# Kernel tuning notes

Hardware: AMD Instinct MI355X
Metric: run time of the kernel (lower is better)

## Reference

```python
import jax, jax.numpy as jnp
import numpy as np


def setup_inputs() -> dict:
    key = jax.random.key(0)
    ks = jax.random.split(key, 4)
    T, B, E = 2048, 2, 1024
    query = jax.random.normal(ks[0], (T, B, E), dtype=jnp.float32)
    attn_mask = jnp.zeros((T, T), dtype=jnp.float32)
    Wqkv = jax.random.normal(ks[1], (3 * E, E), dtype=jnp.float32) * 0.02
    bqkv = jnp.zeros((3 * E,), dtype=jnp.float32)
    Wout = jax.random.normal(ks[2], (E, E), dtype=jnp.float32) * 0.02
    bout = jnp.zeros((E,), dtype=jnp.float32)
    return {"query": query, "attn_mask": attn_mask, "Wqkv": Wqkv,
            "bqkv": bqkv, "Wout": Wout, "bout": bout, "num_heads": 16}


def reference(query, attn_mask, Wqkv, bqkv, Wout, bout, num_heads):
    T, B, E = query.shape
    H = num_heads
    hd = E // H
    scaling = hd ** -0.5
    # fused QKV projection: [T,B,3E]
    qkv = jnp.einsum('tbe,fe->tbf', query, Wqkv) + bqkv
    q, k, v = jnp.split(qkv, 3, axis=-1)
    q = q * scaling
    # [T,B,E] -> [B*H, T, hd]
    def to_heads(x):
        return x.reshape(T, B * H, hd).transpose(1, 0, 2)
    q, k, v = to_heads(q), to_heads(k), to_heads(v)
    # scores [B*H, T, T]
    scores = jnp.einsum('bth,bsh->bts', q, k) + attn_mask[None, :, :]
    probs = jax.nn.softmax(scores, axis=-1)  # dropout p=0
    attn = jnp.einsum('bts,bsh->bth', probs, v)  # [B*H, T, hd]
    attn = attn.transpose(1, 0, 2).reshape(T, B, E)
    out = jnp.einsum('tbe,fe->tbf', attn, Wout) + bout
    avg_w = probs.reshape(B, H, T, T).sum(axis=1) / H
    return out, avg_w
```

## Files before the change

### kernel.cpp

```cpp
#include <hip/hip_runtime.h>
#include <cstdint>
#include <cstddef>

#define Tt 2048
#define Bb 2
#define Ee 1024
#define Hh 16
#define HD 64
#define BHh (Bb*Hh)
#define Mm (Tt*Bb)

typedef short bf16x8 __attribute__((ext_vector_type(8)));
typedef float f32x4  __attribute__((ext_vector_type(4)));

#define MFMA16(a,b,c) __builtin_amdgcn_mfma_f32_16x16x32_bf16(a, b, c, 0, 0, 0)

__device__ __forceinline__ unsigned short f2bf(float f) {
    unsigned int u = __builtin_bit_cast(unsigned int, f);
    u += 0x7FFFu + ((u >> 16) & 1u);
    return (unsigned short)(u >> 16);
}
__device__ __forceinline__ unsigned int pack2bf(float lo, float hi) {
    return (unsigned int)f2bf(lo) | ((unsigned int)f2bf(hi) << 16);
}

__device__ __forceinline__ int swzA(int row, int dwcol) {
    return (row*32 + dwcol) ^ ((row & 7) << 2);
}
__device__ __forceinline__ int swzG(int row, int dwcol) {
    return (row*16 + dwcol) ^ ((row & 3) << 2);
}

__device__ __forceinline__ bf16x8 ldfrag(const unsigned short* base, int row, int col) {
    const unsigned int* p = (const unsigned int*)(base + row*66 + col);
    const unsigned int* q = (const unsigned int*)(base + row*66 + col + 16);
    uint4 u;
    u.x = p[0]; u.y = p[1];
    u.z = q[0]; u.w = q[1];
    return __builtin_bit_cast(bf16x8, u);
}

__global__ __launch_bounds__(256)
void to_bf16(const float* __restrict__ src, unsigned short* __restrict__ dst, int n8)
{
    const int stride = gridDim.x * 256;
    for (int i = blockIdx.x*256 + threadIdx.x; i < n8; i += stride) {
        const float4 a = ((const float4*)src)[2*i];
        const float4 b = ((const float4*)src)[2*i + 1];
        const uint4 u = {pack2bf(a.x,a.y), pack2bf(a.z,a.w),
                         pack2bf(b.x,b.y), pack2bf(b.z,b.w)};
        ((uint4*)dst)[i] = u;
    }
}

template<int MODE>
__global__ __launch_bounds__(256)
void gemm_mfma(const unsigned short* __restrict__ A, const unsigned short* __restrict__ W,
               const float* __restrict__ bias, float* __restrict__ Cout,
               unsigned short* __restrict__ qbuf, unsigned short* __restrict__ kbuf,
               unsigned short* __restrict__ vbuf, int N, int K)
{
    __shared__ __align__(16) unsigned int AsDW[128*16];
    __shared__ __align__(16) unsigned int WsDW[128*16];
    const int tid  = threadIdx.x;
    const int bm   = blockIdx.y * 128;
    const int bn   = blockIdx.x * 128;
    const int w    = tid >> 6;
    const int lane = tid & 63;
    const int lr   = lane & 15;
    const int lg   = lane >> 4;
    const int wm   = (w >> 1) * 64;
    const int wn   = (w & 1) * 64;

    f32x4 acc[4][4];
#pragma unroll
    for (int m = 0; m < 4; ++m)
#pragma unroll
        for (int n = 0; n < 4; ++n)
            acc[m][n] = f32x4{0.f, 0.f, 0.f, 0.f};

    const int r1  = tid >> 2;
    const int cdw = (tid & 3) * 4;

    for (int k0 = 0; k0 < K; k0 += 32) {
        __syncthreads();
        {
            const uint4 a0 = *(const uint4*)&A[(size_t)(bm + r1)      * K + k0 + cdw*2];
            const uint4 a1 = *(const uint4*)&A[(size_t)(bm + r1 + 64) * K + k0 + cdw*2];
            const uint4 w0 = *(const uint4*)&W[(size_t)(bn + r1)      * K + k0 + cdw*2];
            const uint4 w1 = *(const uint4*)&W[(size_t)(bn + r1 + 64) * K + k0 + cdw*2];
            *(uint4*)(AsDW + swzG(r1,      cdw)) = a0;
            *(uint4*)(AsDW + swzG(r1 + 64, cdw)) = a1;
            *(uint4*)(WsDW + swzG(r1,      cdw)) = w0;
            *(uint4*)(WsDW + swzG(r1 + 64, cdw)) = w1;
        }
        __syncthreads();

        bf16x8 af[4], wf[4];
#pragma unroll
        for (int i = 0; i < 4; ++i) {
            af[i] = __builtin_bit_cast(bf16x8, *(const uint4*)(AsDW + swzG(wm + 16*i + lr, 4*lg)));
            wf[i] = __builtin_bit_cast(bf16x8, *(const uint4*)(WsDW + swzG(wn + 16*i + lr, 4*lg)));
        }
#pragma unroll
        for (int m = 0; m < 4; ++m)
#pragma unroll
            for (int n = 0; n < 4; ++n)
                acc[m][n] = MFMA16(af[m], wf[n], acc[m][n]);
    }

#pragma unroll
    for (int nsub = 0; nsub < 4; ++nsub) {
        const int n0 = bn + wn + 16*nsub + lr;
        const float bv = bias[n0];
#pragma unroll
        for (int msub = 0; msub < 4; ++msub) {
#pragma unroll
            for (int reg = 0; reg < 4; ++reg) {
                const int m = bm + wm + 16*msub + 4*lg + reg;
                float v = acc[msub][nsub][reg] + bv;
                if (MODE == 0) {
                    const int which = n0 >> 10;
                    const int e0 = n0 & 1023;
                    const int h = e0 >> 6, d0 = e0 & 63;
                    if (which == 0) v *= 0.125f;
                    unsigned short* dst = (which == 0) ? qbuf : (which == 1) ? kbuf : vbuf;
                    dst[((size_t)((m & 1)*Hh + h) * Tt + (m >> 1)) * HD + d0] = f2bf(v);
                } else {
                    Cout[(size_t)m * N + n0] = v;
                }
            }
        }
    }
}

__global__ __launch_bounds__(512)
void attn_mfma(const unsigned short* __restrict__ qb, const unsigned short* __restrict__ kb,
               const unsigned short* __restrict__ vb, const float* __restrict__ mask,
               unsigned short* __restrict__ attnb, float* __restrict__ lbuf)
{
    __shared__ __align__(16) unsigned int KsDW[2][64*32];
    __shared__ __align__(16) unsigned short Vt[2][64*66];
    __shared__ float l_sh[128];

    const int tid  = threadIdx.x;
    const int bid  = blockIdx.x;
    const int wid  = (bid & 7) * 64 + (bid >> 3);
    const int bh   = wid & 31;
    const int t0   = (wid >> 5) * 128;
    const int w    = tid >> 6;
    const int lane = tid & 63;
    const int lr   = lane & 15;
    const int lg   = lane >> 4;
    const int b = bh >> 4, h = bh & 15;

    const unsigned short* __restrict__ Qg = qb + (size_t)bh * Tt * HD;
    const unsigned short* __restrict__ Kg = kb + (size_t)bh * Tt * HD;
    const unsigned short* __restrict__ Vg = vb + (size_t)bh * Tt * HD;

    const int str = tid >> 3;
    const int sdw = (tid & 7) * 4;

    const int vdg = tid & 15;
    const int vs2 = tid >> 4;

    bf16x8 qf[2];
    for (int half = 0; half < 2; ++half) {
        __syncthreads();
        *(uint4*)(KsDW[0] + swzA(str, sdw)) =
            *(const uint4*)&Qg[(size_t)(t0 + half*64 + str) * HD + sdw*2];
        __syncthreads();
        if ((w >> 2) == half) {
            const int r = 16*(w & 3) + lr;
            qf[0] = __builtin_bit_cast(bf16x8, *(const uint4*)(KsDW[0] + swzA(r, 4*lg)));
            qf[1] = __builtin_bit_cast(bf16x8, *(const uint4*)(KsDW[0] + swzA(r, 16 + 4*lg)));
        }
    }

    f32x4 oacc[4];
#pragma unroll
    for (int d = 0; d < 4; ++d)
        oacc[d] = f32x4{0.f, 0.f, 0.f, 0.f};
    float lacc = 0.f;

    {
        const uint4 k0r = *(const uint4*)&Kg[(size_t)str * HD + sdw*2];
        const uint2 a0  = *(const uint2*)&Vg[(size_t)(2*vs2)     * HD + vdg*4];
        const uint2 c0  = *(const uint2*)&Vg[(size_t)(2*vs2 + 1) * HD + vdg*4];
        __syncthreads();
        *(uint4*)(KsDW[0] + swzA(str, sdw)) = k0r;
        unsigned short* vt0 = &Vt[0][0];
        *(unsigned int*)&vt0[(vdg*4+0)*66 + 2*vs2] = (a0.x & 0xFFFFu) | (c0.x << 16);
        *(unsigned int*)&vt0[(vdg*4+1)*66 + 2*vs2] = (a0.x >> 16)     | (c0.x & 0xFFFF0000u);
        *(unsigned int*)&vt0[(vdg*4+2)*66 + 2*vs2] = (a0.y & 0xFFFFu) | (c0.y << 16);
        *(unsigned int*)&vt0[(vdg*4+3)*66 + 2*vs2] = (a0.y >> 16)     | (c0.y & 0xFFFF0000u);
        __syncthreads();
    }

    int cur = 0;
    for (int s0 = 0; s0 < Tt; s0 += 64) {
        const bool has_next = (s0 + 64 < Tt);
        uint4 kn; uint2 van, vcn;
        if (has_next) {
            kn  = *(const uint4*)&Kg[(size_t)(s0 + 64 + str) * HD + sdw*2];
            van = *(const uint2*)&Vg[(size_t)(s0 + 64 + 2*vs2)     * HD + vdg*4];
            vcn = *(const uint2*)&Vg[(size_t)(s0 + 64 + 2*vs2 + 1) * HD + vdg*4];
        }

        const unsigned int* Kc = KsDW[cur];
        const unsigned short* Vc = &Vt[cur][0];

        f32x4 sacc[4];
#pragma unroll
        for (int ssub = 0; ssub < 4; ++ssub) {
            const bf16x8 a0 = __builtin_bit_cast(bf16x8,
                *(const uint4*)(Kc + swzA(16*ssub + lr, 4*lg)));
            const bf16x8 a1 = __builtin_bit_cast(bf16x8,
                *(const uint4*)(Kc + swzA(16*ssub + lr, 16 + 4*lg)));
            f32x4 z = {0.f, 0.f, 0.f, 0.f};
            z = MFMA16(a0, qf[0], z);
            z = MFMA16(a1, qf[1], z);
            sacc[ssub] = z;
        }

        unsigned int pw[8];
        {
            float lt = 0.f;
            const float* __restrict__ mrow =
                &mask[(size_t)(t0 + 16*w + lr) * Tt + s0];
#pragma unroll
            for (int ssub = 0; ssub < 4; ++ssub) {
                const float4 mv = *(const float4*)&mrow[16*ssub + 4*lg];
                const float e0 = __expf(sacc[ssub][0] + mv.x);
                const float e1 = __expf(sacc[ssub][1] + mv.y);
                const float e2 = __expf(sacc[ssub][2] + mv.z);
                const float e3 = __expf(sacc[ssub][3] + mv.w);
                lt += (e0 + e1) + (e2 + e3);
                pw[ssub*2]     = pack2bf(e0, e1);
                pw[ssub*2 + 1] = pack2bf(e2, e3);
            }
            lt += __shfl_xor(lt, 16);
            lt += __shfl_xor(lt, 32);
            lacc += lt;
        }

        const uint4 ua = {pw[0], pw[1], pw[2], pw[3]};
        const uint4 ub = {pw[4], pw[5], pw[6], pw[7]};
#pragma unroll
        for (int dsub = 0; dsub < 4; ++dsub) {
            const bf16x8 b0 = ldfrag(Vc, 16*dsub + lr, 4*lg);
            const bf16x8 b1 = ldfrag(Vc, 16*dsub + lr, 32 + 4*lg);
            oacc[dsub] = MFMA16(__builtin_bit_cast(bf16x8, ua), b0, oacc[dsub]);
            oacc[dsub] = MFMA16(__builtin_bit_cast(bf16x8, ub), b1, oacc[dsub]);
        }

        if (has_next) {
            *(uint4*)(KsDW[cur ^ 1] + swzA(str, sdw)) = kn;
            unsigned short* vt1 = &Vt[cur ^ 1][0];
            *(unsigned int*)&vt1[(vdg*4+0)*66 + 2*vs2] = (van.x & 0xFFFFu) | (vcn.x << 16);
            *(unsigned int*)&vt1[(vdg*4+1)*66 + 2*vs2] = (van.x >> 16)     | (vcn.x & 0xFFFF0000u);
            *(unsigned int*)&vt1[(vdg*4+2)*66 + 2*vs2] = (van.y & 0xFFFFu) | (vcn.y << 16);
            *(unsigned int*)&vt1[(vdg*4+3)*66 + 2*vs2] = (van.y >> 16)     | (vcn.y & 0xFFFF0000u);
        }
        __syncthreads();
        cur ^= 1;
    }

    if (lg == 0) l_sh[16*w + lr] = lacc;
    __syncthreads();
#pragma unroll
    for (int reg = 0; reg < 4; ++reg) {
        const int tl = 16*w + 4*lg + reg;
        const float inv = 1.f / l_sh[tl];
        const int t = t0 + tl;
#pragma unroll
        for (int dsub = 0; dsub < 4; ++dsub)
            attnb[((size_t)t * Bb + b) * Ee + h*HD + dsub*16 + lr] =
                f2bf(oacc[dsub][reg] * inv);
    }
    if (lg == 0)
        lbuf[(size_t)bh * Tt + t0 + 16*w + lr] = lacc;
}

__global__ __launch_bounds__(256)
void avg_probs_mfma(const unsigned short* __restrict__ qb, const unsigned short* __restrict__ kb,
                    const float* __restrict__ mask, const float* __restrict__ lbuf,
                    float* __restrict__ avg)
{
    __shared__ unsigned short Qs[64][66];
    __shared__ unsigned short Ksh[64][66];
    __shared__ float linv[16][64];

    const int tid  = threadIdx.x;
    const int b    = blockIdx.z;
    const int t0   = blockIdx.y * 64;
    const int s0   = blockIdx.x * 64;
    const int w    = tid >> 6;
    const int lane = tid & 63;
    const int lr   = lane & 15;
    const int lg   = lane >> 4;

    {
        const int h = tid >> 4, tl = (tid & 15) * 4;
        const float4 lv = *(const float4*)&lbuf[(size_t)(b*Hh + h) * Tt + t0 + tl];
        linv[h][tl+0] = 1.f / (16.f * lv.x);
        linv[h][tl+1] = 1.f / (16.f * lv.y);
        linv[h][tl+2] = 1.f / (16.f * lv.z);
        linv[h][tl+3] = 1.f / (16.f * lv.w);
    }

    f32x4 mf[4];
#pragma unroll
    for (int ssub = 0; ssub < 4; ++ssub)
#pragma unroll
        for (int reg = 0; reg < 4; ++reg)
            mf[ssub][reg] = mask[(size_t)(t0 + 16*w + 4*lg + reg) * Tt + s0 + 16*ssub + lr];

    f32x4 av[4];
#pragma unroll
    for (int ssub = 0; ssub < 4; ++ssub) av[ssub] = f32x4{0.f, 0.f, 0.f, 0.f};

    const int str = tid >> 2;
    const int stc = (tid & 3) * 16;

    for (int h = 0; h < Hh; ++h) {
        const unsigned short* __restrict__ Qg = qb + (size_t)(b*Hh + h) * Tt * HD;
        const unsigned short* __restrict__ Kg = kb + (size_t)(b*Hh + h) * Tt * HD;
        __syncthreads();
        {
            const unsigned short* Qp = &Qg[(size_t)(t0 + str) * HD + stc];
            const unsigned short* Kp = &Kg[(size_t)(s0 + str) * HD + stc];
            const uint4 q0 = *(const uint4*)Qp;
            const uint4 q1 = *(const uint4*)(Qp + 8);
            const uint4 k0 = *(const uint4*)Kp;
            const uint4 k1 = *(const uint4*)(Kp + 8);
            *(uint4*)&Qs[str][stc]      = q0;
            *(uint4*)&Qs[str][stc + 8]  = q1;
            *(uint4*)&Ksh[str][stc]     = k0;
            *(uint4*)&Ksh[str][stc + 8] = k1;
        }
        __syncthreads();

        const float lv0 = linv[h][16*w + 4*lg + 0];
        const float lv1 = linv[h][16*w + 4*lg + 1];
        const float lv2 = linv[h][16*w + 4*lg + 2];
        const float lv3 = linv[h][16*w + 4*lg + 3];

        const bf16x8 af0 = ldfrag(&Qs[0][0], 16*w + lr, 4*lg);
        const bf16x8 af1 = ldfrag(&Qs[0][0], 16*w + lr, 32 + 4*lg);
#pragma unroll
        for (int ssub = 0; ssub < 4; ++ssub) {
            const bf16x8 bf0 = ldfrag(&Ksh[0][0], 16*ssub + lr, 4*lg);
            const bf16x8 bf1 = ldfrag(&Ksh[0][0], 16*ssub + lr, 32 + 4*lg);
            f32x4 z = {0.f, 0.f, 0.f, 0.f};
            z = MFMA16(af0, bf0, z);
            z = MFMA16(af1, bf1, z);
            av[ssub][0] += __expf(z[0] + mf[ssub][0]) * lv0;
            av[ssub][1] += __expf(z[1] + mf[ssub][1]) * lv1;
            av[ssub][2] += __expf(z[2] + mf[ssub][2]) * lv2;
            av[ssub][3] += __expf(z[3] + mf[ssub][3]) * lv3;
        }
    }

#pragma unroll
    for (int ssub = 0; ssub < 4; ++ssub)
#pragma unroll
        for (int reg = 0; reg < 4; ++reg)
            avg[((size_t)b * Tt + t0 + 16*w + 4*lg + reg) * Tt + s0 + 16*ssub + lr] =
                av[ssub][reg];
}

extern "C" void kernel_launch(void* const* d_in, const int* in_sizes, int n_in,
                              void* d_out, int out_size, void* d_ws, size_t ws_size,
                              hipStream_t stream)
{
    (void)in_sizes; (void)n_in; (void)out_size; (void)ws_size;
    const float* query = (const float*)d_in[0];
    const float* mask  = (const float*)d_in[1];
    const float* Wqkv  = (const float*)d_in[2];
    const float* bqkv  = (const float*)d_in[3];
    const float* Wout  = (const float*)d_in[4];
    const float* bout  = (const float*)d_in[5];

    float* out = (float*)d_out;
    float* avg = out + (size_t)Tt * Bb * Ee;

    const size_t S1 = (size_t)BHh * Tt * HD;
    unsigned short* wsu     = (unsigned short*)d_ws;
    unsigned short* qbuf    = wsu;
    unsigned short* kbuf    = qbuf + S1;
    unsigned short* vbuf    = kbuf + S1;
    unsigned short* attnb   = vbuf + S1;
    unsigned short* querybf = attnb + (size_t)Mm * Ee;
    unsigned short* wqkvbf  = querybf + (size_t)Mm * Ee;
    unsigned short* woutbf  = wqkvbf + (size_t)3 * Ee * Ee;
    float*          lbuf    = (float*)(woutbf + (size_t)Ee * Ee);

    to_bf16<<<1024, 256, 0, stream>>>(query, querybf, (Mm*Ee)/8);
    to_bf16<<<1024, 256, 0, stream>>>(Wqkv, wqkvbf, (3*Ee*Ee)/8);
    to_bf16<<<512,  256, 0, stream>>>(Wout, woutbf, (Ee*Ee)/8);

    gemm_mfma<0><<<dim3(3072/128, Mm/128), 256, 0, stream>>>(
        querybf, wqkvbf, bqkv, nullptr, qbuf, kbuf, vbuf, 3072, Ee);
    attn_mfma<<<dim3(BHh * (Tt/128)), 512, 0, stream>>>(
        qbuf, kbuf, vbuf, mask, attnb, lbuf);
    avg_probs_mfma<<<dim3(Tt/64, Tt/64, Bb), 256, 0, stream>>>(
        qbuf, kbuf, mask, lbuf, avg);
    gemm_mfma<1><<<dim3(Ee/128, Mm/128), 256, 0, stream>>>(
        attnb, woutbf, bout, out, nullptr, nullptr, nullptr, Ee, Ee);
}
```

Before: 213.7 us.

## Double-buffer GEMM shared-memory tiles with register prefetch of next K slice

The GEMM now keeps two LDS buffers per operand. It issues the global loads for the next K slice into registers before running the MFMAs on the current slice, then writes them into the other buffer, so each iteration needs one barrier instead of two. The goal is to hide global load latency behind the matrix math. This doubles LDS use and raises register pressure from the prefetch registers, which could lower occupancy.

```diff
diff --git a/kernel.cpp b/kernel.cpp
--- a/kernel.cpp
+++ b/kernel.cpp
@@ -60,8 +60,8 @@
                unsigned short* __restrict__ qbuf, unsigned short* __restrict__ kbuf,
                unsigned short* __restrict__ vbuf, int N, int K)
 {
-    __shared__ __align__(16) unsigned int AsDW[128*16];
-    __shared__ __align__(16) unsigned int WsDW[128*16];
+    __shared__ __align__(16) unsigned int AsDW[2][128*16];
+    __shared__ __align__(16) unsigned int WsDW[2][128*16];
     const int tid  = threadIdx.x;
     const int bm   = blockIdx.y * 128;
     const int bn   = blockIdx.x * 128;
@@ -82,31 +82,51 @@
     const int r1  = tid >> 2;
     const int cdw = (tid & 3) * 4;
 
+    {
+        const uint4 a0 = *(const uint4*)&A[(size_t)(bm + r1)      * K + cdw*2];
+        const uint4 a1 = *(const uint4*)&A[(size_t)(bm + r1 + 64) * K + cdw*2];
+        const uint4 w0 = *(const uint4*)&W[(size_t)(bn + r1)      * K + cdw*2];
+        const uint4 w1 = *(const uint4*)&W[(size_t)(bn + r1 + 64) * K + cdw*2];
+        *(uint4*)(AsDW[0] + swzG(r1,      cdw)) = a0;
+        *(uint4*)(AsDW[0] + swzG(r1 + 64, cdw)) = a1;
+        *(uint4*)(WsDW[0] + swzG(r1,      cdw)) = w0;
+        *(uint4*)(WsDW[0] + swzG(r1 + 64, cdw)) = w1;
+        __syncthreads();
+    }
+
+    int cur = 0;
     for (int k0 = 0; k0 < K; k0 += 32) {
-        __syncthreads();
-        {
-            const uint4 a0 = *(const uint4*)&A[(size_t)(bm + r1)      * K + k0 + cdw*2];
-            const uint4 a1 = *(const uint4*)&A[(size_t)(bm + r1 + 64) * K + k0 + cdw*2];
-            const uint4 w0 = *(const uint4*)&W[(size_t)(bn + r1)      * K + k0 + cdw*2];
-            const uint4 w1 = *(const uint4*)&W[(size_t)(bn + r1 + 64) * K + k0 + cdw*2];
-            *(uint4*)(AsDW + swzG(r1,      cdw)) = a0;
-            *(uint4*)(AsDW + swzG(r1 + 64, cdw)) = a1;
-            *(uint4*)(WsDW + swzG(r1,      cdw)) = w0;
-            *(uint4*)(WsDW + swzG(r1 + 64, cdw)) = w1;
-        }
-        __syncthreads();
-
+        const bool has_next = (k0 + 32 < K);
+        uint4 an0, an1, wn0, wn1;
+        if (has_next) {
+            an0 = *(const uint4*)&A[(size_t)(bm + r1)      * K + k0 + 32 + cdw*2];
+            an1 = *(const uint4*)&A[(size_t)(bm + r1 + 64) * K + k0 + 32 + cdw*2];
+            wn0 = *(const uint4*)&W[(size_t)(bn + r1)      * K + k0 + 32 + cdw*2];
+            wn1 = *(const uint4*)&W[(size_t)(bn + r1 + 64) * K + k0 + 32 + cdw*2];
+        }
+
+        const unsigned int* Ac = AsDW[cur];
+        const unsigned int* Wc = WsDW[cur];
         bf16x8 af[4], wf[4];
 #pragma unroll
         for (int i = 0; i < 4; ++i) {
-            af[i] = __builtin_bit_cast(bf16x8, *(const uint4*)(AsDW + swzG(wm + 16*i + lr, 4*lg)));
-            wf[i] = __builtin_bit_cast(bf16x8, *(const uint4*)(WsDW + swzG(wn + 16*i + lr, 4*lg)));
+            af[i] = __builtin_bit_cast(bf16x8, *(const uint4*)(Ac + swzG(wm + 16*i + lr, 4*lg)));
+            wf[i] = __builtin_bit_cast(bf16x8, *(const uint4*)(Wc + swzG(wn + 16*i + lr, 4*lg)));
         }
 #pragma unroll
         for (int m = 0; m < 4; ++m)
 #pragma unroll
             for (int n = 0; n < 4; ++n)
                 acc[m][n] = MFMA16(af[m], wf[n], acc[m][n]);
+
+        if (has_next) {
+            *(uint4*)(AsDW[cur ^ 1] + swzG(r1,      cdw)) = an0;
+            *(uint4*)(AsDW[cur ^ 1] + swzG(r1 + 64, cdw)) = an1;
+            *(uint4*)(WsDW[cur ^ 1] + swzG(r1,      cdw)) = wn0;
+            *(uint4*)(WsDW[cur ^ 1] + swzG(r1 + 64, cdw)) = wn1;
+        }
+        __syncthreads();
+        cur ^= 1;
     }
 
 #pragma unroll
```

Result: faster. 202.2 us (-5.4%).
